# Kernel tuning notes

Hardware: AMD Instinct MI355X
Metric: run time of the kernel (lower is better)

The kernel has to match this reference:

```python
import jax, jax.numpy as jnp
import numpy as np

N_NODES = 100000
N_EDGES = 1600000
ATOM_EMB = 64
BOND_EMB = 16
MSG_DIM = 64
OUT_HIDDEN = 128
N_MOLS = 2048
MSG_PASSES = 4


def setup_inputs() -> dict:
    key = jax.random.key(0)
    ks = jax.random.split(key, 16)
    x = jax.random.randint(ks[0], (N_NODES,), 0, 119)
    edge_attr = jax.random.randint(ks[1], (N_EDGES,), 0, 4)
    edge_index = jax.random.randint(ks[2], (2, N_EDGES), 0, N_NODES)
    batch = jnp.sort(jax.random.randint(ks[3], (N_NODES,), 0, N_MOLS))
    s = 0.02
    atom_table = jax.random.normal(ks[4], (119, ATOM_EMB), jnp.float32) * s
    bond_table = jax.random.normal(ks[5], (4, BOND_EMB), jnp.float32) * s
    Wi = jax.random.normal(ks[6], (ATOM_EMB + BOND_EMB, MSG_DIM), jnp.float32) * s
    bi = jnp.zeros((MSG_DIM,), jnp.float32)
    Wu = jax.random.normal(ks[7], (ATOM_EMB + BOND_EMB + MSG_DIM, MSG_DIM), jnp.float32) * s
    bu = jnp.zeros((MSG_DIM,), jnp.float32)
    W1 = jax.random.normal(ks[8], (MSG_DIM, OUT_HIDDEN), jnp.float32) * s
    b1 = jnp.zeros((OUT_HIDDEN,), jnp.float32)
    W2 = jax.random.normal(ks[9], (OUT_HIDDEN, 1), jnp.float32) * s
    b2 = jnp.zeros((1,), jnp.float32)
    return {"x": x, "edge_attr": edge_attr, "edge_index": edge_index, "batch": batch,
            "atom_table": atom_table, "bond_table": bond_table,
            "Wi": Wi, "bi": bi, "Wu": Wu, "bu": bu,
            "W1": W1, "b1": b1, "W2": W2, "b2": b2}


def reference(x, edge_attr, edge_index, batch, atom_table, bond_table, Wi, bi, Wu, bu, W1, b1, W2, b2):
    atom = atom_table[x]                      # [N, ATOM_EMB]
    bond = bond_table[edge_attr]              # [E, BOND_EMB]
    src, dst = edge_index[0], edge_index[1]
    atom_src = atom[src]                      # [E, ATOM_EMB]
    ab = jnp.concatenate([atom_src, bond], axis=1)
    msg = jax.nn.relu(ab @ Wi + bi)           # [E, MSG_DIM]
    for _ in range(MSG_PASSES):
        agg = jax.ops.segment_sum(msg, dst, num_segments=N_NODES)  # [N, MSG_DIM]
        upd_in = jnp.concatenate([ab, agg[src]], axis=1)           # [E, 144]
        msg = jax.nn.relu(upd_in @ Wu + bu)
    node_state = jax.ops.segment_sum(msg, dst, num_segments=N_NODES)
    mol_state = jax.ops.segment_sum(node_state, batch, num_segments=N_MOLS)
    h = jax.nn.relu(mol_state @ W1 + b1)
    return (h @ W2 + b2).squeeze(-1)          # [N_MOLS]
```

## Files before the change

### kernel.cpp

```cpp
#include <hip/hip_runtime.h>

#define MSG 64
#define SLICE_SHIFT 10
#define MAXSLICES 128
#define REP 8
#define CAP_R 3072
#define CAP_E 20480
#define CAP_B 16384
#define NBIN 64

typedef _Float16 h2 __attribute__((ext_vector_type(2)));
typedef _Float16 h4 __attribute__((ext_vector_type(4)));
typedef _Float16 h8 __attribute__((ext_vector_type(8)));

__device__ inline h8 relu8(h8 v) {
    h8 z = {};
    return __builtin_elementwise_max(v, z);
}

__device__ inline h2 u2h(unsigned u) { union { unsigned u; h2 h; } c; c.u = u; return c.h; }

__global__ void setup_kernel(const float* __restrict__ atom, const float* __restrict__ bond,
                             const float* __restrict__ Wi, const float* __restrict__ bi,
                             const float* __restrict__ Wu, const float* __restrict__ bu,
                             const float* __restrict__ Wagg,
                             _Float16* __restrict__ tAi, _Float16* __restrict__ tBi,
                             _Float16* __restrict__ tAu, _Float16* __restrict__ tBu,
                             unsigned* __restrict__ wst, int* __restrict__ gcur,
                             int AR, int K, int ab) {
    int b = blockIdx.x;
    if (b < 2 * ab + 2) {
        bool upd = b >= ab + 1;
        const float* W = upd ? Wu : Wi;
        int lb = upd ? b - (ab + 1) : b;
        if (lb < ab) {
            _Float16* tA = upd ? tAu : tAi;
            int t = lb * 256 + threadIdx.x;
            if (t < AR * MSG) {
                int i = t & 63, a = t >> 6;
                float s = 0.f;
                for (int k = 0; k < 64; ++k) s = fmaf(atom[a * 64 + k], W[k * 64 + i], s);
                tA[t] = (_Float16)s;
            }
        } else {
            _Float16* tBo = upd ? tBu : tBi;
            const float* bias = upd ? bu : bi;
            const float* W16 = W + 64 * MSG;
            int t = threadIdx.x;
            int i = t & 63, r = t >> 6;
            float s = bias[i];
            for (int k = 0; k < 16; ++k) s = fmaf(bond[r * 16 + k], W16[k * 64 + i], s);
            tBo[t] = (_Float16)s;
        }
    } else if (b < 2 * ab + 10) {
        int t = (b - (2 * ab + 2)) * 256 + threadIdx.x;
        if (t < 2048) {
            int k2 = t >> 6, c = t & 63;
            h2 h; h[0] = (_Float16)Wagg[(2 * k2) * 64 + c]; h[1] = (_Float16)Wagg[(2 * k2 + 1) * 64 + c];
            union { h2 h; unsigned u; } cv; cv.h = h;
            wst[k2 * 64 + c] = cv.u;
        }
    } else {
        for (int q = threadIdx.x; q < K * REP; q += 256) gcur[q] = q * CAP_R;
    }
}

__global__ void node_init_kernel(const int* __restrict__ x, const _Float16* __restrict__ tA,
                                 _Float16* __restrict__ bufC, int N) {
    int t = blockIdx.x * blockDim.x + threadIdx.x;
    int v = t >> 3, j = t & 7;
    if (v < N) ((h8*)bufC)[(long long)v * 8 + j] = ((const h8*)tA)[x[v] * 8 + j];
}

__global__ __launch_bounds__(256) void partition_kernel(
    const int* __restrict__ ei, const int* __restrict__ eattr,
    int E, int* __restrict__ gcur, unsigned long long* __restrict__ aux, int K)
{
    __shared__ int cnt[MAXSLICES];
    __shared__ int base[MAXSLICES];
    if (threadIdx.x < MAXSLICES) cnt[threadIdx.x] = 0;
    __syncthreads();
    int rep = blockIdx.x & (REP - 1);
    int e0 = blockIdx.x * 1024;
    int sl0 = -1, sl1 = -1, sl2 = -1, sl3 = -1;
    int rk0 = 0, rk1 = 0, rk2 = 0, rk3 = 0;
    unsigned long long p0 = 0, p1 = 0, p2 = 0, p3 = 0;
    {
        int e = e0 + 0 * 256 + threadIdx.x;
        if (e < E) {
            int s = ei[e], d = ei[E + e];
            p0 = ((unsigned long long)((unsigned)s | ((unsigned)eattr[e] << 17)) << 17) | (unsigned)d;
            sl0 = d >> SLICE_SHIFT; rk0 = atomicAdd(&cnt[sl0], 1);
        }
    }
    {
        int e = e0 + 1 * 256 + threadIdx.x;
        if (e < E) {
            int s = ei[e], d = ei[E + e];
            p1 = ((unsigned long long)((unsigned)s | ((unsigned)eattr[e] << 17)) << 17) | (unsigned)d;
            sl1 = d >> SLICE_SHIFT; rk1 = atomicAdd(&cnt[sl1], 1);
        }
    }
    {
        int e = e0 + 2 * 256 + threadIdx.x;
        if (e < E) {
            int s = ei[e], d = ei[E + e];
            p2 = ((unsigned long long)((unsigned)s | ((unsigned)eattr[e] << 17)) << 17) | (unsigned)d;
            sl2 = d >> SLICE_SHIFT; rk2 = atomicAdd(&cnt[sl2], 1);
        }
    }
    {
        int e = e0 + 3 * 256 + threadIdx.x;
        if (e < E) {
            int s = ei[e], d = ei[E + e];
            p3 = ((unsigned long long)((unsigned)s | ((unsigned)eattr[e] << 17)) << 17) | (unsigned)d;
            sl3 = d >> SLICE_SHIFT; rk3 = atomicAdd(&cnt[sl3], 1);
        }
    }
    __syncthreads();
    if (threadIdx.x < K && cnt[threadIdx.x] > 0)
        base[threadIdx.x] = atomicAdd(&gcur[threadIdx.x * REP + rep], cnt[threadIdx.x]);
    __syncthreads();
    if (sl0 >= 0) aux[base[sl0] + rk0] = p0;
    if (sl1 >= 0) aux[base[sl1] + rk1] = p1;
    if (sl2 >= 0) aux[base[sl2] + rk2] = p2;
    if (sl3 >= 0) aux[base[sl3] + rk3] = p3;
}

__global__ __launch_bounds__(1024) void place_kernel(
    const unsigned long long* __restrict__ aux, const int* __restrict__ gcur,
    int* __restrict__ nstart, int* __restrict__ ndeg,
    unsigned* __restrict__ packed, int N)
{
    __shared__ int cnt[1 << SLICE_SHIFT];
    __shared__ int wsum[16];
    int s = blockIdx.x;
    int lo = s << SLICE_SHIFT;
    cnt[threadIdx.x] = 0;
    __syncthreads();
    for (int r = 0; r < REP; ++r) {
        int q = s * REP + r;
        int start = q * CAP_R, end = gcur[q];
        for (int idx = start + threadIdx.x; idx < end; idx += 1024)
            atomicAdd(&cnt[(int)(aux[idx] & 0x1FFFFu) & ((1 << SLICE_SHIFT) - 1)], 1);
    }
    __syncthreads();
    int c = cnt[threadIdx.x];
    int lane = threadIdx.x & 63, w = threadIdx.x >> 6;
    int sc = c;
    for (int off = 1; off < 64; off <<= 1) { int t = __shfl_up(sc, off); if (lane >= off) sc += t; }
    if (lane == 63) wsum[w] = sc;
    __syncthreads();
    if (w == 0 && lane < 16) {
        int t = wsum[lane];
        for (int off = 1; off < 16; off <<= 1) { int u = __shfl_up(t, off); if (lane >= off) t += u; }
        wsum[lane] = t;
    }
    __syncthreads();
    if (w > 0) sc += wsum[w - 1];
    int v = lo + threadIdx.x;
    int st = s * CAP_E + sc - c;
    if (v < N) { nstart[v] = st; ndeg[v] = c; }
    __syncthreads();
    cnt[threadIdx.x] = st;
    __syncthreads();
    for (int r = 0; r < REP; ++r) {
        int q = s * REP + r;
        int start = q * CAP_R, end = gcur[q];
        for (int idx = start + threadIdx.x; idx < end; idx += 1024) {
            unsigned long long a = aux[idx];
            int d = (int)(a & 0x1FFFFu);
            unsigned pw = (unsigned)(a >> 17);
            int p = atomicAdd(&cnt[d & ((1 << SLICE_SHIFT) - 1)], 1);
            packed[p] = pw;
        }
    }
}

__global__ __launch_bounds__(256) void dbin_kernel(const int* __restrict__ ndeg, int N,
                                                   int* __restrict__ bcnt, int* __restrict__ bucket) {
    __shared__ int cnt[NBIN];
    __shared__ int base[NBIN];
    if (threadIdx.x < NBIN) cnt[threadIdx.x] = 0;
    __syncthreads();
    int v = blockIdx.x * 256 + threadIdx.x;
    int b = -1, rk = 0;
    if (v < N) { b = min(ndeg[v], NBIN - 1); rk = atomicAdd(&cnt[b], 1); }
    __syncthreads();
    if (threadIdx.x < NBIN && cnt[threadIdx.x] > 0)
        base[threadIdx.x] = atomicAdd(&bcnt[threadIdx.x], cnt[threadIdx.x]);
    __syncthreads();
    if (b >= 0) bucket[b * CAP_B + base[b] + rk] = v;
}

__global__ void compact_kernel(const int* __restrict__ bucket, const int* __restrict__ bcnt,
                               const int* __restrict__ nstart, const int* __restrict__ ndeg,
                               int2* __restrict__ srt) {
    __shared__ int sbase;
    int b = blockIdx.x;
    if (threadIdx.x == 0) {
        int run = 0;
        for (int i = 0; i < b; ++i) run += bcnt[i];
        sbase = run;
    }
    __syncthreads();
    int n = bcnt[b], base = sbase;
    for (int i = threadIdx.x; i < n; i += 256) {
        int v = bucket[b * CAP_B + i];
        srt[base + i] = make_int2(nstart[v], v | (ndeg[v] << 17));
    }
}

template <bool FINAL>
__global__ __launch_bounds__(256, 8) void gather_kernel(
    const unsigned* __restrict__ packed, const int2* __restrict__ srt,
    const _Float16* __restrict__ nodearr, const _Float16* __restrict__ tB,
    const unsigned* __restrict__ wst_g, const _Float16* __restrict__ tAu,
    const int* __restrict__ x, _Float16* __restrict__ out, int N)
{
    __shared__ _Float16 tbs[4 * 64];
    __shared__ unsigned wst[32 * 64];
    __shared__ _Float16 rowb[32][72];
    tbs[threadIdx.x] = tB[threadIdx.x];
    if (!FINAL)
        for (int idx = threadIdx.x; idx < 2048; idx += 256) wst[idx] = wst_g[idx];
    __syncthreads();
    int t = blockIdx.x * 256 + threadIdx.x;
    int vi = t >> 3;
    int j = threadIdx.x & 7;
    int w = threadIdx.x >> 3;
    const h8* na8 = (const h8*)nodearr;
    const _Float16* tbsj = tbs + j * 8;
    h8 acc = {};
    int v = 0;
    bool valid = vi < N;
    if (valid) {
        int2 s2 = srt[vi];
        int e = s2.x;
        v = (int)((unsigned)s2.y & 0x1FFFFu);
        int end = e + (int)((unsigned)s2.y >> 17);
        for (; e + 7 < end; e += 8) {
            unsigned q0 = packed[e],     q1 = packed[e + 1], q2 = packed[e + 2], q3 = packed[e + 3];
            unsigned q4 = packed[e + 4], q5 = packed[e + 5], q6 = packed[e + 6], q7 = packed[e + 7];
            h8 m0 = na8[(q0 & 0x1FFFFu) * 8 + j];
            h8 m1 = na8[(q1 & 0x1FFFFu) * 8 + j];
            h8 m2 = na8[(q2 & 0x1FFFFu) * 8 + j];
            h8 m3 = na8[(q3 & 0x1FFFFu) * 8 + j];
            h8 m4 = na8[(q4 & 0x1FFFFu) * 8 + j];
            h8 m5 = na8[(q5 & 0x1FFFFu) * 8 + j];
            h8 m6 = na8[(q6 & 0x1FFFFu) * 8 + j];
            h8 m7 = na8[(q7 & 0x1FFFFu) * 8 + j];
            h8 t0 = *(const h8*)&tbsj[(q0 >> 17) * 64];
            h8 t1 = *(const h8*)&tbsj[(q1 >> 17) * 64];
            h8 t2 = *(const h8*)&tbsj[(q2 >> 17) * 64];
            h8 t3 = *(const h8*)&tbsj[(q3 >> 17) * 64];
            h8 t4 = *(const h8*)&tbsj[(q4 >> 17) * 64];
            h8 t5 = *(const h8*)&tbsj[(q5 >> 17) * 64];
            h8 t6 = *(const h8*)&tbsj[(q6 >> 17) * 64];
            h8 t7 = *(const h8*)&tbsj[(q7 >> 17) * 64];
            h8 s0 = relu8(m0 + t0), s1 = relu8(m1 + t1);
            h8 s2v = relu8(m2 + t2), s3 = relu8(m3 + t3);
            h8 s4 = relu8(m4 + t4), s5 = relu8(m5 + t5);
            h8 s6 = relu8(m6 + t6), s7 = relu8(m7 + t7);
            acc += ((s0 + s1) + (s2v + s3)) + ((s4 + s5) + (s6 + s7));
        }
        for (; e < end; ++e) {
            unsigned q0 = packed[e];
            h8 m0 = na8[(q0 & 0x1FFFFu) * 8 + j];
            h8 t0 = *(const h8*)&tbsj[(q0 >> 17) * 64];
            acc += relu8(m0 + t0);
        }
    }
    if (FINAL) {
        if (valid) ((h8*)out)[(long long)v * 8 + j] = acc;
        return;
    }
    *(h8*)&rowb[w][j * 8] = acc;
    __syncthreads();
    if (!valid) return;
    const h2* rp = (const h2*)&rowb[w][0];
    const unsigned* wj = wst + j * 8;
    float o0 = 0.f, o1 = 0.f, o2 = 0.f, o3 = 0.f, o4 = 0.f, o5 = 0.f, o6 = 0.f, o7 = 0.f;
#pragma unroll
    for (int k2 = 0; k2 < 32; ++k2) {
        h2 r = rp[k2];
        uint4 wa = *(const uint4*)&wj[k2 * 64];
        uint4 wb = *(const uint4*)&wj[k2 * 64 + 4];
        o0 = __builtin_amdgcn_fdot2(r, u2h(wa.x), o0, false);
        o1 = __builtin_amdgcn_fdot2(r, u2h(wa.y), o1, false);
        o2 = __builtin_amdgcn_fdot2(r, u2h(wa.z), o2, false);
        o3 = __builtin_amdgcn_fdot2(r, u2h(wa.w), o3, false);
        o4 = __builtin_amdgcn_fdot2(r, u2h(wb.x), o4, false);
        o5 = __builtin_amdgcn_fdot2(r, u2h(wb.y), o5, false);
        o6 = __builtin_amdgcn_fdot2(r, u2h(wb.z), o6, false);
        o7 = __builtin_amdgcn_fdot2(r, u2h(wb.w), o7, false);
    }
    h8 ta = ((const h8*)tAu)[x[v] * 8 + j];
    h8 o;
    o[0] = (_Float16)(o0 + (float)ta[0]); o[1] = (_Float16)(o1 + (float)ta[1]);
    o[2] = (_Float16)(o2 + (float)ta[2]); o[3] = (_Float16)(o3 + (float)ta[3]);
    o[4] = (_Float16)(o4 + (float)ta[4]); o[5] = (_Float16)(o5 + (float)ta[5]);
    o[6] = (_Float16)(o6 + (float)ta[6]); o[7] = (_Float16)(o7 + (float)ta[7]);
    ((h8*)out)[(long long)v * 8 + j] = o;
}

__global__ void mol_pool_kernel(const _Float16* __restrict__ ns, const int* __restrict__ batch,
                                float* __restrict__ mol, int N) {
    int g = (blockIdx.x * blockDim.x + threadIdx.x) >> 4;
    int j = threadIdx.x & 15;
    int n0 = g * 32;
    if (n0 >= N) return;
    int n1 = min(n0 + 32, N);
    const h4* ns4 = (const h4*)ns;
    int cur = batch[n0];
    float ax = 0.f, ay = 0.f, az = 0.f, aw = 0.f;
    for (int n = n0; n < n1; ++n) {
        int b = batch[n];
        if (b != cur) {
            float* mp = &mol[(long long)cur * 64 + j * 4];
            atomicAdd(mp + 0, ax); atomicAdd(mp + 1, ay);
            atomicAdd(mp + 2, az); atomicAdd(mp + 3, aw);
            ax = ay = az = aw = 0.f; cur = b;
        }
        h4 vv = ns4[(long long)n * 16 + j];
        ax += (float)vv.x; ay += (float)vv.y; az += (float)vv.z; aw += (float)vv.w;
    }
    float* mp = &mol[(long long)cur * 64 + j * 4];
    atomicAdd(mp + 0, ax); atomicAdd(mp + 1, ay);
    atomicAdd(mp + 2, az); atomicAdd(mp + 3, aw);
}

__global__ void head_kernel(const float* __restrict__ mol, const float* __restrict__ W1,
                            const float* __restrict__ b1, const float* __restrict__ W2,
                            const float* __restrict__ b2, float* __restrict__ out) {
    int g = blockIdx.x;
    int j = threadIdx.x;
    float s = b1[j];
#pragma unroll
    for (int k = 0; k < 64; ++k) s = fmaf(mol[g * 64 + k], W1[k * 128 + j], s);
    s = fmaxf(s, 0.0f) * W2[j];
    __shared__ float red[128];
    red[j] = s;
    __syncthreads();
    for (int off = 64; off > 0; off >>= 1) {
        if (j < off) red[j] += red[j + off];
        __syncthreads();
    }
    if (j == 0) out[g] = red[0] + b2[0];
}

extern "C" void kernel_launch(void* const* d_in, const int* in_sizes, int n_in,
                              void* d_out, int out_size, void* d_ws, size_t ws_size,
                              hipStream_t stream) {
    const int*   x          = (const int*)d_in[0];
    const int*   eattr      = (const int*)d_in[1];
    const int*   ei         = (const int*)d_in[2];
    const int*   batch      = (const int*)d_in[3];
    const float* atom_table = (const float*)d_in[4];
    const float* bond_table = (const float*)d_in[5];
    const float* Wi         = (const float*)d_in[6];
    const float* bi         = (const float*)d_in[7];
    const float* Wu         = (const float*)d_in[8];
    const float* bu         = (const float*)d_in[9];
    const float* W1         = (const float*)d_in[10];
    const float* b1         = (const float*)d_in[11];
    const float* W2         = (const float*)d_in[12];
    const float* b2         = (const float*)d_in[13];

    const int N = in_sizes[0];
    const int E = in_sizes[1];
    const int M = out_size;
    const int AR = in_sizes[4] / 64;
    const int K = (N + (1 << SLICE_SHIFT) - 1) >> SLICE_SHIFT;
    const int ab = (AR * MSG + 255) / 256;

    char* ws = (char*)d_ws;
    size_t off_b = 0;
    auto alloc = [&](size_t bytes) -> void* {
        void* p = ws + off_b;
        off_b = (off_b + bytes + 255) & ~(size_t)255;
        return p;
    };
    size_t nbytes = (size_t)N * MSG * 2;
    size_t abytes = (size_t)K * REP * CAP_R * 8;
    _Float16* bufA  = (_Float16*)alloc(nbytes);
    _Float16* bufB  = (_Float16*)alloc(nbytes > abytes ? nbytes : abytes);
    _Float16* bufC  = (_Float16*)alloc(nbytes);
    unsigned long long* aux = (unsigned long long*)bufB;
    unsigned* packed = (unsigned*)alloc((size_t)K * CAP_E * 4);
    int*      nstart = (int*)alloc((size_t)N * 4);
    int*      ndeg   = (int*)alloc((size_t)N * 4);
    int2*     srt    = (int2*)alloc((size_t)N * 8);
    int*      bucket = (int*)alloc((size_t)NBIN * CAP_B * 4);
    int*      bcnt   = (int*)alloc((size_t)NBIN * 4);
    int*      gcur   = (int*)alloc((size_t)MAXSLICES * REP * 4);
    _Float16* tAi    = (_Float16*)alloc((size_t)AR * MSG * 2);
    _Float16* tBi    = (_Float16*)alloc((size_t)4 * MSG * 2);
    _Float16* tAu    = (_Float16*)alloc((size_t)AR * MSG * 2);
    _Float16* tBu    = (_Float16*)alloc((size_t)4 * MSG * 2);
    unsigned* wstb   = (unsigned*)alloc((size_t)32 * 64 * 4);
    float*    mol    = (float*)alloc((size_t)M * MSG * 4);
    (void)ws_size; (void)n_in;

    const float* Wagg = Wu + 80 * MSG;

    setup_kernel<<<2 * ab + 11, 256, 0, stream>>>(atom_table, bond_table, Wi, bi, Wu, bu, Wagg,
                                                  tAi, tBi, tAu, tBu, wstb, gcur, AR, K, ab);
    node_init_kernel<<<(int)(((long long)N * 8 + 255) / 256), 256, 0, stream>>>(x, tAi, bufC, N);

    partition_kernel<<<(E + 1023) / 1024, 256, 0, stream>>>(ei, eattr, E, gcur, aux, K);
    place_kernel<<<K, 1024, 0, stream>>>(aux, gcur, nstart, ndeg, packed, N);

    hipMemsetAsync(bcnt, 0, (size_t)NBIN * 4, stream);
    dbin_kernel<<<(N + 255) / 256, 256, 0, stream>>>(ndeg, N, bcnt, bucket);
    compact_kernel<<<NBIN, 256, 0, stream>>>(bucket, bcnt, nstart, ndeg, srt);

    const int gblocks = (int)(((long long)N * 8 + 255) / 256);
    gather_kernel<false><<<gblocks, 256, 0, stream>>>(packed, srt, bufC, tBi, wstb, tAu, x, bufA, N);
    gather_kernel<false><<<gblocks, 256, 0, stream>>>(packed, srt, bufA, tBu, wstb, tAu, x, bufB, N);
    gather_kernel<false><<<gblocks, 256, 0, stream>>>(packed, srt, bufB, tBu, wstb, tAu, x, bufA, N);
    gather_kernel<false><<<gblocks, 256, 0, stream>>>(packed, srt, bufA, tBu, wstb, tAu, x, bufB, N);
    gather_kernel<true><<<gblocks, 256, 0, stream>>>(packed, srt, bufB, tBu, nullptr, nullptr, nullptr, bufA, N);

    hipMemsetAsync(mol, 0, (size_t)M * MSG * 4, stream);
    mol_pool_kernel<<<(((N + 31) / 32) * 16 + 255) / 256, 256, 0, stream>>>(bufA, batch, mol, N);
    head_kernel<<<M, 128, 0, stream>>>(mol, W1, b1, W2, b2, (float*)d_out);
}
```

Measured before the change: 304.3 us.

## Stage partition/place scatters in LDS, halve slice size, fold memsets into setup

```diff
diff --git a/kernel.cpp b/kernel.cpp
--- a/kernel.cpp
+++ b/kernel.cpp
@@ -1,11 +1,12 @@
 #include <hip/hip_runtime.h>
 
 #define MSG 64
-#define SLICE_SHIFT 10
-#define MAXSLICES 128
+#define SLICE_SHIFT 9
+#define SLICE_N (1 << SLICE_SHIFT)
+#define MAXSLICES 256
 #define REP 8
-#define CAP_R 3072
-#define CAP_E 20480
+#define CAP_R 1536
+#define CAP_E 12288
 #define CAP_B 16384
 #define NBIN 64
 
@@ -27,6 +28,7 @@
                              _Float16* __restrict__ tAi, _Float16* __restrict__ tBi,
                              _Float16* __restrict__ tAu, _Float16* __restrict__ tBu,
                              unsigned* __restrict__ wst, int* __restrict__ gcur,
+                             int* __restrict__ bcnt, float* __restrict__ mol,
                              int AR, int K, int ab) {
     int b = blockIdx.x;
     if (b < 2 * ab + 2) {
@@ -60,8 +62,12 @@
             union { h2 h; unsigned u; } cv; cv.h = h;
             wst[k2 * 64 + c] = cv.u;
         }
+    } else if (b == 2 * ab + 10) {
+        for (int q = threadIdx.x; q < K * REP; q += 256) gcur[q] = q * CAP_R;
+        if (threadIdx.x < NBIN) bcnt[threadIdx.x] = 0;
     } else {
-        for (int q = threadIdx.x; q < K * REP; q += 256) gcur[q] = q * CAP_R;
+        int t = (b - (2 * ab + 11)) * 256 + threadIdx.x;
+        ((float4*)mol)[t] = make_float4(0.f, 0.f, 0.f, 0.f);
     }
 }
 
@@ -77,54 +83,55 @@
     int E, int* __restrict__ gcur, unsigned long long* __restrict__ aux, int K)
 {
     __shared__ int cnt[MAXSLICES];
-    __shared__ int base[MAXSLICES];
+    __shared__ int lexcl[MAXSLICES];
+    __shared__ int gbase[MAXSLICES];
+    __shared__ int wsum[4];
+    __shared__ unsigned long long stage[1024];
     if (threadIdx.x < MAXSLICES) cnt[threadIdx.x] = 0;
     __syncthreads();
     int rep = blockIdx.x & (REP - 1);
     int e0 = blockIdx.x * 1024;
-    int sl0 = -1, sl1 = -1, sl2 = -1, sl3 = -1;
-    int rk0 = 0, rk1 = 0, rk2 = 0, rk3 = 0;
-    unsigned long long p0 = 0, p1 = 0, p2 = 0, p3 = 0;
-    {
-        int e = e0 + 0 * 256 + threadIdx.x;
+    int total = min(1024, E - e0);
+    int sl[4]; int rk[4]; unsigned long long rec[4];
+#pragma unroll
+    for (int r = 0; r < 4; ++r) {
+        sl[r] = -1;
+        int e = e0 + r * 256 + threadIdx.x;
         if (e < E) {
             int s = ei[e], d = ei[E + e];
-            p0 = ((unsigned long long)((unsigned)s | ((unsigned)eattr[e] << 17)) << 17) | (unsigned)d;
-            sl0 = d >> SLICE_SHIFT; rk0 = atomicAdd(&cnt[sl0], 1);
-        }
-    }
+            rec[r] = ((unsigned long long)((unsigned)s | ((unsigned)eattr[e] << 17)) << 17) | (unsigned)d;
+            sl[r] = d >> SLICE_SHIFT;
+            rk[r] = atomicAdd(&cnt[sl[r]], 1);
+        }
+    }
+    __syncthreads();
     {
-        int e = e0 + 1 * 256 + threadIdx.x;
-        if (e < E) {
-            int s = ei[e], d = ei[E + e];
-            p1 = ((unsigned long long)((unsigned)s | ((unsigned)eattr[e] << 17)) << 17) | (unsigned)d;
-            sl1 = d >> SLICE_SHIFT; rk1 = atomicAdd(&cnt[sl1], 1);
-        }
-    }
-    {
-        int e = e0 + 2 * 256 + threadIdx.x;
-        if (e < E) {
-            int s = ei[e], d = ei[E + e];
-            p2 = ((unsigned long long)((unsigned)s | ((unsigned)eattr[e] << 17)) << 17) | (unsigned)d;
-            sl2 = d >> SLICE_SHIFT; rk2 = atomicAdd(&cnt[sl2], 1);
-        }
-    }
-    {
-        int e = e0 + 3 * 256 + threadIdx.x;
-        if (e < E) {
-            int s = ei[e], d = ei[E + e];
-            p3 = ((unsigned long long)((unsigned)s | ((unsigned)eattr[e] << 17)) << 17) | (unsigned)d;
-            sl3 = d >> SLICE_SHIFT; rk3 = atomicAdd(&cnt[sl3], 1);
-        }
-    }
-    __syncthreads();
-    if (threadIdx.x < K && cnt[threadIdx.x] > 0)
-        base[threadIdx.x] = atomicAdd(&gcur[threadIdx.x * REP + rep], cnt[threadIdx.x]);
-    __syncthreads();
-    if (sl0 >= 0) aux[base[sl0] + rk0] = p0;
-    if (sl1 >= 0) aux[base[sl1] + rk1] = p1;
-    if (sl2 >= 0) aux[base[sl2] + rk2] = p2;
-    if (sl3 >= 0) aux[base[sl3] + rk3] = p3;
+        int c = cnt[threadIdx.x];
+        int lane = threadIdx.x & 63, w = threadIdx.x >> 6;
+        int sc = c;
+        for (int off = 1; off < 64; off <<= 1) { int t = __shfl_up(sc, off); if (lane >= off) sc += t; }
+        if (lane == 63) wsum[w] = sc;
+        __syncthreads();
+        int add = 0;
+        for (int q = 0; q < 3; ++q) if (w > q) add += wsum[q];
+        lexcl[threadIdx.x] = sc + add - c;
+        if (threadIdx.x < K && c > 0)
+            gbase[threadIdx.x] = atomicAdd(&gcur[threadIdx.x * REP + rep], c);
+    }
+    __syncthreads();
+#pragma unroll
+    for (int r = 0; r < 4; ++r)
+        if (sl[r] >= 0) stage[lexcl[sl[r]] + rk[r]] = rec[r];
+    __syncthreads();
+#pragma unroll
+    for (int r = 0; r < 4; ++r) {
+        int i = r * 256 + threadIdx.x;
+        if (i < total) {
+            unsigned long long a = stage[i];
+            int s = (int)((unsigned)a & 0x1FFFFu) >> SLICE_SHIFT;
+            aux[gbase[s] + (i - lexcl[s])] = a;
+        }
+    }
 }
 
 __global__ __launch_bounds__(1024) void place_kernel(
@@ -132,37 +139,40 @@
     int* __restrict__ nstart, int* __restrict__ ndeg,
     unsigned* __restrict__ packed, int N)
 {
-    __shared__ int cnt[1 << SLICE_SHIFT];
-    __shared__ int wsum[16];
+    __shared__ int cnt[SLICE_N];
+    __shared__ int wsum[8];
+    __shared__ unsigned stage[CAP_E];
     int s = blockIdx.x;
     int lo = s << SLICE_SHIFT;
-    cnt[threadIdx.x] = 0;
+    if (threadIdx.x < SLICE_N) cnt[threadIdx.x] = 0;
     __syncthreads();
     for (int r = 0; r < REP; ++r) {
         int q = s * REP + r;
         int start = q * CAP_R, end = gcur[q];
         for (int idx = start + threadIdx.x; idx < end; idx += 1024)
-            atomicAdd(&cnt[(int)(aux[idx] & 0x1FFFFu) & ((1 << SLICE_SHIFT) - 1)], 1);
-    }
-    __syncthreads();
-    int c = cnt[threadIdx.x];
-    int lane = threadIdx.x & 63, w = threadIdx.x >> 6;
-    int sc = c;
-    for (int off = 1; off < 64; off <<= 1) { int t = __shfl_up(sc, off); if (lane >= off) sc += t; }
-    if (lane == 63) wsum[w] = sc;
-    __syncthreads();
-    if (w == 0 && lane < 16) {
-        int t = wsum[lane];
-        for (int off = 1; off < 16; off <<= 1) { int u = __shfl_up(t, off); if (lane >= off) t += u; }
-        wsum[lane] = t;
-    }
-    __syncthreads();
-    if (w > 0) sc += wsum[w - 1];
-    int v = lo + threadIdx.x;
-    int st = s * CAP_E + sc - c;
-    if (v < N) { nstart[v] = st; ndeg[v] = c; }
-    __syncthreads();
-    cnt[threadIdx.x] = st;
+            atomicAdd(&cnt[(int)(aux[idx] & 0x1FFFFu) & (SLICE_N - 1)], 1);
+    }
+    __syncthreads();
+    int c = 0, sc = 0;
+    if (threadIdx.x < SLICE_N) {
+        c = cnt[threadIdx.x];
+        int lane = threadIdx.x & 63, w = threadIdx.x >> 6;
+        sc = c;
+        for (int off = 1; off < 64; off <<= 1) { int t = __shfl_up(sc, off); if (lane >= off) sc += t; }
+        if (lane == 63) wsum[w] = sc;
+    }
+    __syncthreads();
+    int totale = 0;
+    if (threadIdx.x < SLICE_N) {
+        int w = threadIdx.x >> 6;
+        int add = 0;
+        for (int q = 0; q < 7; ++q) if (w > q) add += wsum[q];
+        sc += add;
+        int v = lo + threadIdx.x;
+        if (v < N) { nstart[v] = s * CAP_E + sc - c; ndeg[v] = c; }
+    }
+    __syncthreads();
+    if (threadIdx.x < SLICE_N) cnt[threadIdx.x] = sc - c;
     __syncthreads();
     for (int r = 0; r < REP; ++r) {
         int q = s * REP + r;
@@ -170,11 +180,14 @@
         for (int idx = start + threadIdx.x; idx < end; idx += 1024) {
             unsigned long long a = aux[idx];
             int d = (int)(a & 0x1FFFFu);
-            unsigned pw = (unsigned)(a >> 17);
-            int p = atomicAdd(&cnt[d & ((1 << SLICE_SHIFT) - 1)], 1);
-            packed[p] = pw;
-        }
-    }
+            int p = atomicAdd(&cnt[d & (SLICE_N - 1)], 1);
+            stage[p] = (unsigned)(a >> 17);
+        }
+    }
+    __syncthreads();
+    totale = cnt[SLICE_N - 1];
+    for (int i = threadIdx.x; i < totale; i += 1024)
+        packed[s * CAP_E + i] = stage[i];
 }
 
 __global__ __launch_bounds__(256) void dbin_kernel(const int* __restrict__ ndeg, int N,
@@ -371,7 +384,7 @@
     const int E = in_sizes[1];
     const int M = out_size;
     const int AR = in_sizes[4] / 64;
-    const int K = (N + (1 << SLICE_SHIFT) - 1) >> SLICE_SHIFT;
+    const int K = (N + SLICE_N - 1) >> SLICE_SHIFT;
     const int ab = (AR * MSG + 255) / 256;
 
     char* ws = (char*)d_ws;
@@ -393,7 +406,7 @@
     int2*     srt    = (int2*)alloc((size_t)N * 8);
     int*      bucket = (int*)alloc((size_t)NBIN * CAP_B * 4);
     int*      bcnt   = (int*)alloc((size_t)NBIN * 4);
-    int*      gcur   = (int*)alloc((size_t)MAXSLICES * REP * 4);
+    int*      gcur   = (int*)alloc((size_t)K * REP * 4);
     _Float16* tAi    = (_Float16*)alloc((size_t)AR * MSG * 2);
     _Float16* tBi    = (_Float16*)alloc((size_t)4 * MSG * 2);
     _Float16* tAu    = (_Float16*)alloc((size_t)AR * MSG * 2);
@@ -404,14 +417,14 @@
 
     const float* Wagg = Wu + 80 * MSG;
 
-    setup_kernel<<<2 * ab + 11, 256, 0, stream>>>(atom_table, bond_table, Wi, bi, Wu, bu, Wagg,
-                                                  tAi, tBi, tAu, tBu, wstb, gcur, AR, K, ab);
+    setup_kernel<<<2 * ab + 11 + 128, 256, 0, stream>>>(atom_table, bond_table, Wi, bi, Wu, bu, Wagg,
+                                                        tAi, tBi, tAu, tBu, wstb, gcur, bcnt, mol,
+                                                        AR, K, ab);
     node_init_kernel<<<(int)(((long long)N * 8 + 255) / 256), 256, 0, stream>>>(x, tAi, bufC, N);
 
     partition_kernel<<<(E + 1023) / 1024, 256, 0, stream>>>(ei, eattr, E, gcur, aux, K);
     place_kernel<<<K, 1024, 0, stream>>>(aux, gcur, nstart, ndeg, packed, N);
 
-    hipMemsetAsync(bcnt, 0, (size_t)NBIN * 4, stream);
     dbin_kernel<<<(N + 255) / 256, 256, 0, stream>>>(ndeg, N, bcnt, bucket);
     compact_kernel<<<NBIN, 256, 0, stream>>>(bucket, bcnt, nstart, ndeg, srt);
 
@@ -422,7 +435,6 @@
     gather_kernel<false><<<gblocks, 256, 0, stream>>>(packed, srt, bufA, tBu, wstb, tAu, x, bufB, N);
     gather_kernel<true><<<gblocks, 256, 0, stream>>>(packed, srt, bufB, tBu, nullptr, nullptr, nullptr, bufA, N);
 
-    hipMemsetAsync(mol, 0, (size_t)M * MSG * 4, stream);
     mol_pool_kernel<<<(((N + 31) / 32) * 16 + 255) / 256, 256, 0, stream>>>(bufA, batch, mol, N);
     head_kernel<<<M, 128, 0, stream>>>(mol, W1, b1, W2, b2, (float*)d_out);
 }
```

Measured after the change: 287.0 us. 5.7% less time.
